# Optimization experiments

Hardware: AMD Instinct MI355X
Metric: run time of the kernel (lower is better)

Reference implementation:

```python
import jax, jax.numpy as jnp
import numpy as np

HIDDEN = 576
N_HEADS = 9
KV_HEADS = 3
HEAD_DIM = HIDDEN // N_HEADS  # 64
ROPE_BASE = 10000.0
B, S = 2, 4096


def rotate_half(x):
    x1, x2 = jnp.split(x, 2, axis=-1)
    return jnp.concatenate((-x2, x1), axis=-1)


def rope_cos_sin(seq_len, dim, base):
    freq = 1.0 / base ** (jnp.arange(0, dim, 2, dtype=jnp.float32) / dim)
    angles = jnp.arange(seq_len, dtype=jnp.float32)[:, None] * freq[None, :]  # [S, dim/2]
    emb = jnp.concatenate((angles, angles), axis=-1)[None]  # [1, S, dim]
    return jnp.cos(emb), jnp.sin(emb)


def setup_inputs() -> dict:
    key = jax.random.key(0)
    kx, kq, kk, kv, ko = jax.random.split(key, 5)
    x = jax.random.normal(kx, (B, S, HIDDEN), dtype=jnp.float32)
    sc = 1.0 / np.sqrt(HIDDEN)
    Wq = jax.random.normal(kq, (HIDDEN, N_HEADS * HEAD_DIM), dtype=jnp.float32) * sc
    Wk = jax.random.normal(kk, (HIDDEN, KV_HEADS * HEAD_DIM), dtype=jnp.float32) * sc
    Wv = jax.random.normal(kv, (HIDDEN, KV_HEADS * HEAD_DIM), dtype=jnp.float32) * sc
    Wo = jax.random.normal(ko, (HIDDEN, HIDDEN), dtype=jnp.float32) * sc
    causal = jnp.where(jnp.tril(jnp.ones((S, S), dtype=bool)), 0.0, -1e9).astype(jnp.float32)
    attention_mask = jnp.broadcast_to(causal[None, None], (B, 1, S, S))
    return {"x": x, "attention_mask": attention_mask, "Wq": Wq, "Wk": Wk, "Wv": Wv, "Wo": Wo}


def reference(x, attention_mask, Wq, Wk, Wv, Wo):
    b, s, _ = x.shape
    n_rep = N_HEADS // KV_HEADS
    # projections -> [b, heads, s, d]
    q = (x @ Wq).reshape(b, s, N_HEADS, HEAD_DIM).transpose(0, 2, 1, 3)
    k = (x @ Wk).reshape(b, s, KV_HEADS, HEAD_DIM).transpose(0, 2, 1, 3)
    v = (x @ Wv).reshape(b, s, KV_HEADS, HEAD_DIM).transpose(0, 2, 1, 3)
    cos, sin = rope_cos_sin(s, HEAD_DIM, ROPE_BASE)
    cos, sin = cos[:, None], sin[:, None]  # unsqueeze head dim -> [1,1,s,d]
    q = q * cos + rotate_half(q) * sin
    k = k * cos + rotate_half(k) * sin
    # repeat_kv expansion
    k = jnp.repeat(k, n_rep, axis=1)
    v = jnp.repeat(v, n_rep, axis=1)
    scores = jnp.einsum('bhqd,bhkd->bhqk', q, k) / jnp.sqrt(jnp.float32(HEAD_DIM))
    scores = scores + attention_mask
    attn = jax.nn.softmax(scores, axis=-1)
    out = jnp.einsum('bhqk,bhkd->bhqd', attn, v)
    out = out.transpose(0, 2, 1, 3).reshape(b, s, HIDDEN)
    return out @ Wo
```

## Files before the change

kernel.cpp:

```cpp
#include <hip/hip_runtime.h>
#include <hip/hip_bf16.h>
#include <math.h>

#define HID 576
#define NHEADS 9
#define KVHEADS 3
#define HD 64
#define SEQ 4096
#define NBATCH 2

typedef __attribute__((ext_vector_type(8))) short short8;
typedef __attribute__((ext_vector_type(4))) float f32x4;
typedef __attribute__((ext_vector_type(16))) float f32x16;
typedef __attribute__((ext_vector_type(4))) unsigned int u32x4;

#define EXP2F(x) exp2f(x)

#define QSCALE 0.18033688011112042f

#define NBH (NBATCH*NHEADS)
#define NPAIR 64

__device__ __forceinline__ unsigned short f2bf(float f){
  unsigned int u = __float_as_uint(f);
  u += 0x7FFFu + ((u >> 16) & 1u);
  return (unsigned short)(u >> 16);
}
__device__ __forceinline__ float bf2f(unsigned short u){
  return __uint_as_float(((unsigned)u) << 16);
}

__device__ __forceinline__ unsigned cvt_pk_bf16(float lo, float hi){
  unsigned r;
  asm("v_cvt_pk_bf16_f32 %0, %1, %2" : "=v"(r) : "v"(lo), "v"(hi));
  return r;
}

__global__ __launch_bounds__(256) void k_cast(const float* __restrict__ x,
                                              unsigned short* __restrict__ xb, int n){
  int i = (blockIdx.x * 256 + threadIdx.x) * 4;
  if (i < n){
    float4 v = *(const float4*)(x + i);
    ushort4 o;
    o.x = f2bf(v.x); o.y = f2bf(v.y); o.z = f2bf(v.z); o.w = f2bf(v.w);
    *(ushort4*)(xb + i) = o;
  }
}

__global__ __launch_bounds__(256) void k_qkv(const unsigned short* __restrict__ xb,
    const float* __restrict__ Wq, const float* __restrict__ Wk, const float* __restrict__ Wv,
    unsigned short* __restrict__ Qo, unsigned short* __restrict__ Ko,
    unsigned short* __restrict__ Vt)
{
  __shared__ unsigned short As[64][40];
  __shared__ unsigned short Bs[64][40];
  const int tn = blockIdx.x;
  const int m0 = blockIdx.y * 64;
  const int t  = threadIdx.x;
  const int w  = t >> 6;
  const int l  = t & 63;
  const int l15 = l & 15, lg = l >> 4;

  const float* W; int nb, ldw;
  if (tn < 9)      { W = Wq; nb = tn * 64;        ldw = 576; }
  else if (tn < 12){ W = Wk; nb = (tn - 9) * 64;  ldw = 192; }
  else             { W = Wv; nb = (tn - 12) * 64; ldw = 192; }

  f32x4 acc[4];
  #pragma unroll
  for (int n = 0; n < 4; ++n){ f32x4 z = {0.f,0.f,0.f,0.f}; acc[n] = z; }

  const int ar = t >> 2, ac = (t & 3) * 8;
  const int bkr = t >> 3, bnc = (t & 7) * 8;

  for (int kt = 0; kt < 18; ++kt){
    const int k0 = kt * 32;
    *(short8*)&As[ar][ac] = *(const short8*)(xb + (m0 + ar) * 576 + k0 + ac);
    {
      const float* src = W + (k0 + bkr) * ldw + nb + bnc;
      float4 v0 = *(const float4*)src;
      float4 v1 = *(const float4*)(src + 4);
      Bs[bnc+0][bkr] = f2bf(v0.x); Bs[bnc+1][bkr] = f2bf(v0.y);
      Bs[bnc+2][bkr] = f2bf(v0.z); Bs[bnc+3][bkr] = f2bf(v0.w);
      Bs[bnc+4][bkr] = f2bf(v1.x); Bs[bnc+5][bkr] = f2bf(v1.y);
      Bs[bnc+6][bkr] = f2bf(v1.z); Bs[bnc+7][bkr] = f2bf(v1.w);
    }
    __syncthreads();
    short8 af = *(const short8*)&As[w*16 + l15][lg*8];
    #pragma unroll
    for (int n = 0; n < 4; ++n){
      short8 bf = *(const short8*)&Bs[n*16 + l15][lg*8];
      acc[n] = __builtin_amdgcn_mfma_f32_16x16x32_bf16(af, bf, acc[n], 0, 0, 0);
    }
    __syncthreads();
  }

  if (tn < 12){
    #pragma unroll
    for (int np = 0; np < 2; ++np){
      const int p = np*16 + l15;
      const float freq = exp2f((float)p * -0.41524101186f);
      #pragma unroll
      for (int reg = 0; reg < 4; ++reg){
        const int grow = m0 + w*16 + lg*4 + reg;
        const int s = grow & (SEQ-1);
        float si, co;
        sincosf((float)s * freq, &si, &co);
        float v0 = acc[np][reg], v1 = acc[np+2][reg];
        acc[np][reg]   = v0*co - v1*si;
        acc[np+2][reg] = v1*co + v0*si;
      }
    }
  }

  if (tn < 9){
    const int h = tn;
    #pragma unroll
    for (int reg = 0; reg < 4; ++reg){
      const int grow = m0 + w*16 + lg*4 + reg;
      const int b = grow >> 12, s = grow & (SEQ-1);
      unsigned short* dst = Qo + ((b*NHEADS + h)*SEQ + s)*64;
      #pragma unroll
      for (int n = 0; n < 4; ++n) dst[n*16 + l15] = f2bf(acc[n][reg] * QSCALE);
    }
  } else if (tn < 12){
    const int h = tn - 9;
    #pragma unroll
    for (int reg = 0; reg < 4; ++reg){
      const int grow = m0 + w*16 + lg*4 + reg;
      const int b = grow >> 12, s = grow & (SEQ-1);
      unsigned short* dst = Ko + ((b*KVHEADS + h)*SEQ + s)*64;
      #pragma unroll
      for (int n = 0; n < 4; ++n) dst[n*16 + l15] = f2bf(acc[n][reg]);
    }
  } else {
    const int h = tn - 12;
    #pragma unroll
    for (int reg = 0; reg < 4; ++reg){
      const int grow = m0 + w*16 + lg*4 + reg;
      const int b = grow >> 12, s = grow & (SEQ-1);
      #pragma unroll
      for (int n = 0; n < 4; ++n)
        Vt[((b*KVHEADS + h)*64 + n*16 + l15)*SEQ + s] = f2bf(acc[n][reg]);
    }
  }
}

__global__ __launch_bounds__(64, 2) void k_attn9(const unsigned short* __restrict__ Q,
    const unsigned short* __restrict__ K, const unsigned short* __restrict__ Vt,
    unsigned short* __restrict__ AO,
    unsigned short* __restrict__ PO, float* __restrict__ Pm, float* __restrict__ Pl,
    int CSP)
{
  int rem = blockIdx.x;
  int j = NPAIR - 1;
  int nch;
  for (;;){
    nch = (2*j + 2 + CSP - 1) / CSP;
    const int cnt = NBH * nch;
    if (rem < cnt || j == 0) break;
    rem -= cnt; --j;
  }
  const int bh = rem / nch;
  const int c  = rem % nch;
  const int s0 = c * CSP;
  const int s1 = min(s0 + CSP, 2*j + 2);
  const bool partial = (nch > 1);
  const int slot = blockIdx.x;

  const int b  = bh / NHEADS, h = bh % NHEADS, kvh = h / 3;
  const int l  = threadIdx.x;
  const int q31 = l & 31, half = l >> 5;
  const int qA0 = j*64, qB0 = j*64 + 32;
  const int myqA = qA0 + q31, myqB = qB0 + q31;

  const unsigned short* QpA = Q + ((size_t)(b*NHEADS + h)*SEQ + qA0 + q31)*HD + half*8;
  const short8 qa0 = *(const short8*)(QpA);
  const short8 qa1 = *(const short8*)(QpA + 16);
  const short8 qa2 = *(const short8*)(QpA + 32);
  const short8 qa3 = *(const short8*)(QpA + 48);
  const unsigned short* QpB = QpA + (size_t)32*HD;
  const short8 qb0 = *(const short8*)(QpB);
  const short8 qb1 = *(const short8*)(QpB + 16);
  const short8 qb2 = *(const short8*)(QpB + 32);
  const short8 qb3 = *(const short8*)(QpB + 48);

  const unsigned short* Kp  = K  + (size_t)(b*KVHEADS + kvh)*SEQ*HD + (size_t)q31*HD + half*8;
  const unsigned short* Vp0 = Vt + (size_t)(b*KVHEADS + kvh)*HD*SEQ + (size_t)q31*SEQ + half*8;
  const unsigned short* Vp1 = Vp0 + (size_t)32*SEQ;

  f32x16 aA0 = {}, aA1 = {}, aB0 = {}, aB1 = {};
  float mA = -3e38f, lsA = 0.f, mB = -3e38f, lsB = 0.f;

  const unsigned short* kp0 = Kp + (size_t)(s0*32)*HD;
  short8 ckf0 = *(const short8*)(kp0);
  short8 ckf1 = *(const short8*)(kp0 + 16);
  short8 ckf2 = *(const short8*)(kp0 + 32);
  short8 ckf3 = *(const short8*)(kp0 + 48);

  for (int s = s0; s < s1; ++s){
    const int ks = s*32;

    short8 vf00 = *(const short8*)(Vp0 + ks);
    short8 vf01 = *(const short8*)(Vp0 + ks + 16);
    short8 vf10 = *(const short8*)(Vp1 + ks);
    short8 vf11 = *(const short8*)(Vp1 + ks + 16);

    __builtin_amdgcn_s_setprio(1);
    f32x16 stA = {}, stB = {};
    stA = __builtin_amdgcn_mfma_f32_32x32x16_bf16(ckf0, qa0, stA, 0,0,0);
    stB = __builtin_amdgcn_mfma_f32_32x32x16_bf16(ckf0, qb0, stB, 0,0,0);
    stA = __builtin_amdgcn_mfma_f32_32x32x16_bf16(ckf1, qa1, stA, 0,0,0);
    stB = __builtin_amdgcn_mfma_f32_32x32x16_bf16(ckf1, qb1, stB, 0,0,0);
    stA = __builtin_amdgcn_mfma_f32_32x32x16_bf16(ckf2, qa2, stA, 0,0,0);
    stB = __builtin_amdgcn_mfma_f32_32x32x16_bf16(ckf2, qb2, stB, 0,0,0);
    stA = __builtin_amdgcn_mfma_f32_32x32x16_bf16(ckf3, qa3, stA, 0,0,0);
    stB = __builtin_amdgcn_mfma_f32_32x32x16_bf16(ckf3, qb3, stB, 0,0,0);
    __builtin_amdgcn_s_setprio(0);

    short8 nkf0, nkf1, nkf2, nkf3;
    const bool more = (s + 1 < s1);
    if (more){
      const unsigned short* kp = Kp + (size_t)(ks + 32)*HD;
      nkf0 = *(const short8*)(kp);
      nkf1 = *(const short8*)(kp + 16);
      nkf2 = *(const short8*)(kp + 32);
      nkf3 = *(const short8*)(kp + 48);
    }

    if (s >= 2*j){
      #pragma unroll
      for (int r = 0; r < 16; ++r){
        const int k = ks + (r & 3) + 8*(r >> 2) + 4*half;
        if (k > myqA) stA[r] = -3e38f;
      }
    }
    if (s == 2*j + 1){
      #pragma unroll
      for (int r = 0; r < 16; ++r){
        const int k = ks + (r & 3) + 8*(r >> 2) + 4*half;
        if (k > myqB) stB[r] = -3e38f;
      }
    }

    {
      float a0 = fmaxf(stA[0], stA[1]),  a1 = fmaxf(stA[2], stA[3]);
      float a2 = fmaxf(stA[4], stA[5]),  a3 = fmaxf(stA[6], stA[7]);
      float a4 = fmaxf(stA[8], stA[9]),  a5 = fmaxf(stA[10], stA[11]);
      float a6 = fmaxf(stA[12], stA[13]),a7 = fmaxf(stA[14], stA[15]);
      float b0 = fmaxf(a0, a1), b1 = fmaxf(a2, a3), b2 = fmaxf(a4, a5), b3 = fmaxf(a6, a7);
      float pmax = fmaxf(fmaxf(b0, b1), fmaxf(b2, b3));
      pmax = fmaxf(pmax, __shfl_xor(pmax, 32));
      if (__any(pmax > mA + 8.0f)){
        const float mnew  = fmaxf(mA, pmax);
        const float alpha = EXP2F(mA - mnew);
        mA = mnew;
        lsA *= alpha;
        #pragma unroll
        for (int r = 0; r < 16; ++r){
          const float ar = __shfl(alpha, (r & 3) + 8*(r >> 2) + 4*half);
          aA0[r] *= ar; aA1[r] *= ar;
        }
      }
      float psum = 0.f;
      #pragma unroll
      for (int r = 0; r < 16; ++r){ stA[r] = EXP2F(stA[r] - mA); psum += stA[r]; }
      psum += __shfl_xor(psum, 32);
      lsA += psum;
    }
    {
      float a0 = fmaxf(stB[0], stB[1]),  a1 = fmaxf(stB[2], stB[3]);
      float a2 = fmaxf(stB[4], stB[5]),  a3 = fmaxf(stB[6], stB[7]);
      float a4 = fmaxf(stB[8], stB[9]),  a5 = fmaxf(stB[10], stB[11]);
      float a6 = fmaxf(stB[12], stB[13]),a7 = fmaxf(stB[14], stB[15]);
      float b0 = fmaxf(a0, a1), b1 = fmaxf(a2, a3), b2 = fmaxf(a4, a5), b3 = fmaxf(a6, a7);
      float pmax = fmaxf(fmaxf(b0, b1), fmaxf(b2, b3));
      pmax = fmaxf(pmax, __shfl_xor(pmax, 32));
      if (__any(pmax > mB + 8.0f)){
        const float mnew  = fmaxf(mB, pmax);
        const float alpha = EXP2F(mB - mnew);
        mB = mnew;
        lsB *= alpha;
        #pragma unroll
        for (int r = 0; r < 16; ++r){
          const float ar = __shfl(alpha, (r & 3) + 8*(r >> 2) + 4*half);
          aB0[r] *= ar; aB1[r] *= ar;
        }
      }
      float psum = 0.f;
      #pragma unroll
      for (int r = 0; r < 16; ++r){ stB[r] = EXP2F(stB[r] - mB); psum += stB[r]; }
      psum += __shfl_xor(psum, 32);
      lsB += psum;
    }

    union { u32x4 u; short8 s; } paA0, paA1, paB0, paB1;
    {
      unsigned cA = cvt_pk_bf16(stA[0], stA[1]);
      unsigned cB = cvt_pk_bf16(stA[2], stA[3]);
      unsigned cC = cvt_pk_bf16(stA[4], stA[5]);
      unsigned cD = cvt_pk_bf16(stA[6], stA[7]);
      asm("v_permlane32_swap_b32 %0, %1" : "+v"(cA), "+v"(cC));
      asm("v_permlane32_swap_b32 %0, %1" : "+v"(cB), "+v"(cD));
      paA0.u[0] = cA; paA0.u[1] = cB; paA0.u[2] = cC; paA0.u[3] = cD;
      unsigned eA = cvt_pk_bf16(stA[8],  stA[9]);
      unsigned eB = cvt_pk_bf16(stA[10], stA[11]);
      unsigned eC = cvt_pk_bf16(stA[12], stA[13]);
      unsigned eD = cvt_pk_bf16(stA[14], stA[15]);
      asm("v_permlane32_swap_b32 %0, %1" : "+v"(eA), "+v"(eC));
      asm("v_permlane32_swap_b32 %0, %1" : "+v"(eB), "+v"(eD));
      paA1.u[0] = eA; paA1.u[1] = eB; paA1.u[2] = eC; paA1.u[3] = eD;
    }
    {
      unsigned cA = cvt_pk_bf16(stB[0], stB[1]);
      unsigned cB = cvt_pk_bf16(stB[2], stB[3]);
      unsigned cC = cvt_pk_bf16(stB[4], stB[5]);
      unsigned cD = cvt_pk_bf16(stB[6], stB[7]);
      asm("v_permlane32_swap_b32 %0, %1" : "+v"(cA), "+v"(cC));
      asm("v_permlane32_swap_b32 %0, %1" : "+v"(cB), "+v"(cD));
      paB0.u[0] = cA; paB0.u[1] = cB; paB0.u[2] = cC; paB0.u[3] = cD;
      unsigned eA = cvt_pk_bf16(stB[8],  stB[9]);
      unsigned eB = cvt_pk_bf16(stB[10], stB[11]);
      unsigned eC = cvt_pk_bf16(stB[12], stB[13]);
      unsigned eD = cvt_pk_bf16(stB[14], stB[15]);
      asm("v_permlane32_swap_b32 %0, %1" : "+v"(eA), "+v"(eC));
      asm("v_permlane32_swap_b32 %0, %1" : "+v"(eB), "+v"(eD));
      paB1.u[0] = eA; paB1.u[1] = eB; paB1.u[2] = eC; paB1.u[3] = eD;
    }

    __builtin_amdgcn_s_setprio(1);
    aA0 = __builtin_amdgcn_mfma_f32_32x32x16_bf16(paA0.s, vf00, aA0, 0,0,0);
    aB0 = __builtin_amdgcn_mfma_f32_32x32x16_bf16(paB0.s, vf00, aB0, 0,0,0);
    aA0 = __builtin_amdgcn_mfma_f32_32x32x16_bf16(paA1.s, vf01, aA0, 0,0,0);
    aB0 = __builtin_amdgcn_mfma_f32_32x32x16_bf16(paB1.s, vf01, aB0, 0,0,0);
    aA1 = __builtin_amdgcn_mfma_f32_32x32x16_bf16(paA0.s, vf10, aA1, 0,0,0);
    aB1 = __builtin_amdgcn_mfma_f32_32x32x16_bf16(paB0.s, vf10, aB1, 0,0,0);
    aA1 = __builtin_amdgcn_mfma_f32_32x32x16_bf16(paA1.s, vf11, aA1, 0,0,0);
    aB1 = __builtin_amdgcn_mfma_f32_32x32x16_bf16(paB1.s, vf11, aB1, 0,0,0);
    __builtin_amdgcn_s_setprio(0);

    if (more){ ckf0 = nkf0; ckf1 = nkf1; ckf2 = nkf2; ckf3 = nkf3; }
  }

  if (partial){
    unsigned short* PA = PO + (size_t)(slot*2)   * (32*64);
    unsigned short* PB = PO + (size_t)(slot*2+1) * (32*64);
    #pragma unroll
    for (int r = 0; r < 16; ++r){
      const int rq = (r & 3) + 8*(r >> 2) + 4*half;
      PA[rq*64 + q31]      = f2bf(aA0[r]);
      PA[rq*64 + q31 + 32] = f2bf(aA1[r]);
      PB[rq*64 + q31]      = f2bf(aB0[r]);
      PB[rq*64 + q31 + 32] = f2bf(aB1[r]);
    }
    if (half == 0){
      Pm[(size_t)(slot*2)*32 + q31]   = mA;
      Pl[(size_t)(slot*2)*32 + q31]   = lsA;
      Pm[(size_t)(slot*2+1)*32 + q31] = mB;
      Pl[(size_t)(slot*2+1)*32 + q31] = lsB;
    }
  } else {
    const float liA = 1.0f / lsA, liB = 1.0f / lsB;
    #pragma unroll
    for (int r = 0; r < 16; ++r){
      const int rq = (r & 3) + 8*(r >> 2) + 4*half;
      const float la = __shfl(liA, rq), lb = __shfl(liB, rq);
      const size_t baseA = ((size_t)(b*SEQ + qA0 + rq))*576 + h*64 + q31;
      AO[baseA]      = f2bf(aA0[r] * la);
      AO[baseA + 32] = f2bf(aA1[r] * la);
      const size_t baseB = ((size_t)(b*SEQ + qB0 + rq))*576 + h*64 + q31;
      AO[baseB]      = f2bf(aB0[r] * lb);
      AO[baseB + 32] = f2bf(aB1[r] * lb);
    }
  }
}

__global__ __launch_bounds__(256) void k_comb3(const unsigned short* __restrict__ PO,
    const float* __restrict__ Pm, const float* __restrict__ Pl,
    unsigned short* __restrict__ AO, int CSP)
{
  const int blk = blockIdx.x;
  const int mp = blk >> 1, X = blk & 1;
  const int j  = (NPAIR-1) - mp / NBH;
  const int bh = mp % NBH;
  const int nch = (2*j + 2 + CSP - 1) / CSP;
  int pbase = 0;
  for (int j2 = NPAIR-1; j2 > j; --j2) pbase += NBH * ((2*j2 + 2 + CSP - 1) / CSP);
  pbase += bh * nch;

  const int b = bh / NHEADS, h = bh % NHEADS;
  const int t = threadIdx.x;
  const int row = t >> 3;
  const int dg  = (t & 7) * 8;
  const int q0 = j*64 + 32*X;

  float M = -3e38f;
  for (int cc = 0; cc < nch; ++cc)
    M = fmaxf(M, Pm[(size_t)((pbase + cc)*2 + X)*32 + row]);

  float ls = 0.f;
  float o0=0.f,o1=0.f,o2=0.f,o3=0.f,o4=0.f,o5=0.f,o6=0.f,o7=0.f;
  for (int cc = 0; cc < nch; ++cc){
    const int sid = (pbase + cc)*2 + X;
    const float wc = exp2f(Pm[(size_t)sid*32 + row] - M);
    ls += Pl[(size_t)sid*32 + row] * wc;
    const short8 po = *(const short8*)(PO + (size_t)sid*(32*64) + row*64 + dg);
    o0 += bf2f((unsigned short)po[0]) * wc;
    o1 += bf2f((unsigned short)po[1]) * wc;
    o2 += bf2f((unsigned short)po[2]) * wc;
    o3 += bf2f((unsigned short)po[3]) * wc;
    o4 += bf2f((unsigned short)po[4]) * wc;
    o5 += bf2f((unsigned short)po[5]) * wc;
    o6 += bf2f((unsigned short)po[6]) * wc;
    o7 += bf2f((unsigned short)po[7]) * wc;
  }
  const float li = 1.0f / ls;
  ushort4 w0, w1;
  w0.x = f2bf(o0*li); w0.y = f2bf(o1*li); w0.z = f2bf(o2*li); w0.w = f2bf(o3*li);
  w1.x = f2bf(o4*li); w1.y = f2bf(o5*li); w1.z = f2bf(o6*li); w1.w = f2bf(o7*li);
  unsigned short* dst = AO + ((size_t)(b*SEQ + q0 + row))*576 + h*64 + dg;
  *(ushort4*)(dst)     = w0;
  *(ushort4*)(dst + 4) = w1;
}

__global__ __launch_bounds__(256) void k_oproj(const unsigned short* __restrict__ AO,
    const float* __restrict__ Wo, float* __restrict__ out)
{
  __shared__ unsigned short As[64][40];
  __shared__ unsigned short Bs[64][40];
  const int tn = blockIdx.x;
  const int m0 = blockIdx.y * 64;
  const int t  = threadIdx.x;
  const int w  = t >> 6;
  const int l  = t & 63;
  const int l15 = l & 15, lg = l >> 4;
  const int nb = tn * 64;

  f32x4 acc[4];
  #pragma unroll
  for (int n = 0; n < 4; ++n){ f32x4 z = {0.f,0.f,0.f,0.f}; acc[n] = z; }

  const int ar = t >> 2, ac = (t & 3) * 8;
  const int bkr = t >> 3, bnc = (t & 7) * 8;

  for (int kt = 0; kt < 18; ++kt){
    const int k0 = kt * 32;
    *(short8*)&As[ar][ac] = *(const short8*)(AO + (m0 + ar) * 576 + k0 + ac);
    {
      const float* src = Wo + (k0 + bkr) * 576 + nb + bnc;
      float4 v0 = *(const float4*)src;
      float4 v1 = *(const float4*)(src + 4);
      Bs[bnc+0][bkr] = f2bf(v0.x); Bs[bnc+1][bkr] = f2bf(v0.y);
      Bs[bnc+2][bkr] = f2bf(v0.z); Bs[bnc+3][bkr] = f2bf(v0.w);
      Bs[bnc+4][bkr] = f2bf(v1.x); Bs[bnc+5][bkr] = f2bf(v1.y);
      Bs[bnc+6][bkr] = f2bf(v1.z); Bs[bnc+7][bkr] = f2bf(v1.w);
    }
    __syncthreads();
    short8 af = *(const short8*)&As[w*16 + l15][lg*8];
    #pragma unroll
    for (int n = 0; n < 4; ++n){
      short8 bf = *(const short8*)&Bs[n*16 + l15][lg*8];
      acc[n] = __builtin_amdgcn_mfma_f32_16x16x32_bf16(af, bf, acc[n], 0, 0, 0);
    }
    __syncthreads();
  }

  #pragma unroll
  for (int reg = 0; reg < 4; ++reg){
    const int grow = m0 + w*16 + lg*4 + reg;
    float* dst = out + (size_t)grow * 576 + nb;
    #pragma unroll
    for (int n = 0; n < 4; ++n) dst[n*16 + l15] = acc[n][reg];
  }
}

extern "C" void kernel_launch(void* const* d_in, const int* in_sizes, int n_in,
                              void* d_out, int out_size, void* d_ws, size_t ws_size,
                              hipStream_t stream) {
  const float* x  = (const float*)d_in[0];
  const float* Wq = (const float*)d_in[2];
  const float* Wk = (const float*)d_in[3];
  const float* Wv = (const float*)d_in[4];
  const float* Wo = (const float*)d_in[5];
  float* out = (float*)d_out;

  char* ws = (char*)d_ws;
  const size_t XB_BYTES = (size_t)NBATCH*SEQ*HID*2;
  const size_t Q_BYTES  = (size_t)NBATCH*NHEADS*SEQ*HD*2;
  const size_t K_BYTES  = (size_t)NBATCH*KVHEADS*SEQ*HD*2;
  const size_t V_BYTES  = K_BYTES;
  const size_t BASE     = XB_BYTES + Q_BYTES + K_BYTES + V_BYTES;

  int CSP = 256;
  size_t S = 0;
  {
    const int cands[3] = {20, 40, 64};
    for (int ci = 0; ci < 3; ++ci){
      const int cs = cands[ci];
      size_t s2 = 0;
      for (int j = 0; j < NPAIR; ++j) s2 += (size_t)((2*j + 2 + cs - 1) / cs);
      s2 *= NBH;
      const size_t need = BASE + s2*2*(32*64)*2 + 2*(s2*2*32*4);
      if (ws_size >= need){ CSP = cs; break; }
    }
    size_t s3 = 0;
    for (int j = 0; j < NPAIR; ++j) s3 += (size_t)((2*j + 2 + CSP - 1) / CSP);
    S = s3 * NBH;
  }
  const size_t PO_BYTES = S*2*(32*64)*2;
  const size_t PM_BYTES = S*2*32*4;
  const int jmin = CSP/2;
  const int mpairs = (jmin < NPAIR) ? (NPAIR - jmin)*NBH : 0;

  unsigned short* xb = (unsigned short*)ws;
  unsigned short* Q  = (unsigned short*)(ws + XB_BYTES);
  unsigned short* K  = (unsigned short*)(ws + XB_BYTES + Q_BYTES);
  unsigned short* Vt = (unsigned short*)(ws + XB_BYTES + Q_BYTES + K_BYTES);
  unsigned short* PO = (unsigned short*)(ws + BASE);
  float* Pm = (float*)(ws + BASE + PO_BYTES);
  float* Pl = (float*)(ws + BASE + PO_BYTES + PM_BYTES);
  unsigned short* AO = xb;

  hipLaunchKernelGGL(k_cast, dim3((NBATCH*SEQ*HID)/1024), dim3(256), 0, stream,
                     x, xb, NBATCH*SEQ*HID);
  hipLaunchKernelGGL(k_qkv, dim3(15, (NBATCH*SEQ)/64), dim3(256), 0, stream,
                     xb, Wq, Wk, Wv, Q, K, Vt);
  hipLaunchKernelGGL(k_attn9, dim3((unsigned)S), dim3(64), 0, stream,
                     Q, K, Vt, AO, PO, Pm, Pl, CSP);
  if (mpairs > 0)
    hipLaunchKernelGGL(k_comb3, dim3(mpairs*2), dim3(256), 0, stream, PO, Pm, Pl, AO, CSP);
  hipLaunchKernelGGL(k_oproj, dim3(9, (NBATCH*SEQ)/64), dim3(256), 0, stream,
                     AO, Wo, out);
}
```

Measured before the change: 201.0 us.

## Pre-transpose weights to bf16, fuse x cast into QKV, pack attention waves

A new kernel converts all four weight matrices once per call into transposed bf16 copies, so the QKV and output-projection GEMMs load B tiles with plain vector copies instead of scattered per-element f32-to-bf16 stores into shared memory. The separate x-to-bf16 cast kernel is removed; the QKV kernel now reads f32 x directly and converts it with packed bf16 instructions. The attention kernel is relaunched with four independent wavefronts per 256-thread block instead of one wave per block, cutting block count and scheduling overhead. The cost is an extra weight-transpose launch with strided, uncoalesced reads, and more workspace memory.

After: 488.5 us. 143% more time.

```diff
diff --git a/kernel.cpp b/kernel.cpp
--- a/kernel.cpp
+++ b/kernel.cpp
@@ -36,19 +36,28 @@
   return r;
 }
 
-__global__ __launch_bounds__(256) void k_cast(const float* __restrict__ x,
-                                              unsigned short* __restrict__ xb, int n){
-  int i = (blockIdx.x * 256 + threadIdx.x) * 4;
-  if (i < n){
-    float4 v = *(const float4*)(x + i);
-    ushort4 o;
-    o.x = f2bf(v.x); o.y = f2bf(v.y); o.z = f2bf(v.z); o.w = f2bf(v.w);
-    *(ushort4*)(xb + i) = o;
-  }
-}
-
-__global__ __launch_bounds__(256) void k_qkv(const unsigned short* __restrict__ xb,
-    const float* __restrict__ Wq, const float* __restrict__ Wk, const float* __restrict__ Wv,
+__global__ __launch_bounds__(64) void k_prepw(const float* __restrict__ Wq,
+    const float* __restrict__ Wk, const float* __restrict__ Wv, const float* __restrict__ Wo,
+    unsigned short* __restrict__ WTq, unsigned short* __restrict__ WTk,
+    unsigned short* __restrict__ WTv, unsigned short* __restrict__ WTo)
+{
+  const int r = blockIdx.x;
+  const float* W; unsigned short* WT; int N, n;
+  if (r < 576)      { W = Wq; WT = WTq; N = 576; n = r; }
+  else if (r < 768) { W = Wk; WT = WTk; N = 192; n = r - 576; }
+  else if (r < 960) { W = Wv; WT = WTv; N = 192; n = r - 768; }
+  else              { W = Wo; WT = WTo; N = 576; n = r - 960; }
+  const int t = threadIdx.x;
+  #pragma unroll
+  for (int kk = 0; kk < 9; ++kk){
+    const int k = kk*64 + t;
+    WT[(size_t)n*576 + k] = f2bf(W[(size_t)k*N + n]);
+  }
+}
+
+__global__ __launch_bounds__(256) void k_qkv(const float* __restrict__ x,
+    const unsigned short* __restrict__ WTq, const unsigned short* __restrict__ WTk,
+    const unsigned short* __restrict__ WTv,
     unsigned short* __restrict__ Qo, unsigned short* __restrict__ Ko,
     unsigned short* __restrict__ Vt)
 {
@@ -61,29 +70,29 @@
   const int l  = t & 63;
   const int l15 = l & 15, lg = l >> 4;
 
-  const float* W; int nb, ldw;
-  if (tn < 9)      { W = Wq; nb = tn * 64;        ldw = 576; }
-  else if (tn < 12){ W = Wk; nb = (tn - 9) * 64;  ldw = 192; }
-  else             { W = Wv; nb = (tn - 12) * 64; ldw = 192; }
+  const unsigned short* WT; int nb;
+  if (tn < 9)      { WT = WTq; nb = tn * 64; }
+  else if (tn < 12){ WT = WTk; nb = (tn - 9) * 64; }
+  else             { WT = WTv; nb = (tn - 12) * 64; }
 
   f32x4 acc[4];
   #pragma unroll
   for (int n = 0; n < 4; ++n){ f32x4 z = {0.f,0.f,0.f,0.f}; acc[n] = z; }
 
   const int ar = t >> 2, ac = (t & 3) * 8;
-  const int bkr = t >> 3, bnc = (t & 7) * 8;
+  const int br = t >> 2, bc = (t & 3) * 8;
 
   for (int kt = 0; kt < 18; ++kt){
     const int k0 = kt * 32;
-    *(short8*)&As[ar][ac] = *(const short8*)(xb + (m0 + ar) * 576 + k0 + ac);
     {
-      const float* src = W + (k0 + bkr) * ldw + nb + bnc;
-      float4 v0 = *(const float4*)src;
-      float4 v1 = *(const float4*)(src + 4);
-      Bs[bnc+0][bkr] = f2bf(v0.x); Bs[bnc+1][bkr] = f2bf(v0.y);
-      Bs[bnc+2][bkr] = f2bf(v0.z); Bs[bnc+3][bkr] = f2bf(v0.w);
-      Bs[bnc+4][bkr] = f2bf(v1.x); Bs[bnc+5][bkr] = f2bf(v1.y);
-      Bs[bnc+6][bkr] = f2bf(v1.z); Bs[bnc+7][bkr] = f2bf(v1.w);
+      const float* srcA = x + (size_t)(m0 + ar)*576 + k0 + ac;
+      float4 a0 = *(const float4*)srcA;
+      float4 a1 = *(const float4*)(srcA + 4);
+      u32x4 pk;
+      pk[0] = cvt_pk_bf16(a0.x, a0.y); pk[1] = cvt_pk_bf16(a0.z, a0.w);
+      pk[2] = cvt_pk_bf16(a1.x, a1.y); pk[3] = cvt_pk_bf16(a1.z, a1.w);
+      *(u32x4*)&As[ar][ac] = pk;
+      *(short8*)&Bs[br][bc] = *(const short8*)(WT + (size_t)(nb + br)*576 + k0 + bc);
     }
     __syncthreads();
     short8 af = *(const short8*)&As[w*16 + l15][lg*8];
@@ -146,13 +155,16 @@
   }
 }
 
-__global__ __launch_bounds__(64, 2) void k_attn9(const unsigned short* __restrict__ Q,
+__global__ __launch_bounds__(256, 4) void k_attn10(const unsigned short* __restrict__ Q,
     const unsigned short* __restrict__ K, const unsigned short* __restrict__ Vt,
     unsigned short* __restrict__ AO,
     unsigned short* __restrict__ PO, float* __restrict__ Pm, float* __restrict__ Pl,
-    int CSP)
+    int CSP, int Stotal)
 {
-  int rem = blockIdx.x;
+  const int slot = blockIdx.x * 4 + (threadIdx.x >> 6);
+  if (slot >= Stotal) return;
+
+  int rem = slot;
   int j = NPAIR - 1;
   int nch;
   for (;;){
@@ -166,10 +178,9 @@
   const int s0 = c * CSP;
   const int s1 = min(s0 + CSP, 2*j + 2);
   const bool partial = (nch > 1);
-  const int slot = blockIdx.x;
 
   const int b  = bh / NHEADS, h = bh % NHEADS, kvh = h / 3;
-  const int l  = threadIdx.x;
+  const int l  = threadIdx.x & 63;
   const int q31 = l & 31, half = l >> 5;
   const int qA0 = j*64, qB0 = j*64 + 32;
   const int myqA = qA0 + q31, myqB = qB0 + q31;
@@ -424,7 +435,7 @@
 }
 
 __global__ __launch_bounds__(256) void k_oproj(const unsigned short* __restrict__ AO,
-    const float* __restrict__ Wo, float* __restrict__ out)
+    const unsigned short* __restrict__ WoT, float* __restrict__ out)
 {
   __shared__ unsigned short As[64][40];
   __shared__ unsigned short Bs[64][40];
@@ -441,20 +452,11 @@
   for (int n = 0; n < 4; ++n){ f32x4 z = {0.f,0.f,0.f,0.f}; acc[n] = z; }
 
   const int ar = t >> 2, ac = (t & 3) * 8;
-  const int bkr = t >> 3, bnc = (t & 7) * 8;
 
   for (int kt = 0; kt < 18; ++kt){
     const int k0 = kt * 32;
-    *(short8*)&As[ar][ac] = *(const short8*)(AO + (m0 + ar) * 576 + k0 + ac);
-    {
-      const float* src = Wo + (k0 + bkr) * 576 + nb + bnc;
-      float4 v0 = *(const float4*)src;
-      float4 v1 = *(const float4*)(src + 4);
-      Bs[bnc+0][bkr] = f2bf(v0.x); Bs[bnc+1][bkr] = f2bf(v0.y);
-      Bs[bnc+2][bkr] = f2bf(v0.z); Bs[bnc+3][bkr] = f2bf(v0.w);
-      Bs[bnc+4][bkr] = f2bf(v1.x); Bs[bnc+5][bkr] = f2bf(v1.y);
-      Bs[bnc+6][bkr] = f2bf(v1.z); Bs[bnc+7][bkr] = f2bf(v1.w);
-    }
+    *(short8*)&As[ar][ac] = *(const short8*)(AO + (size_t)(m0 + ar)*576 + k0 + ac);
+    *(short8*)&Bs[ar][ac] = *(const short8*)(WoT + (size_t)(nb + ar)*576 + k0 + ac);
     __syncthreads();
     short8 af = *(const short8*)&As[w*16 + l15][lg*8];
     #pragma unroll
@@ -485,11 +487,14 @@
   float* out = (float*)d_out;
 
   char* ws = (char*)d_ws;
-  const size_t XB_BYTES = (size_t)NBATCH*SEQ*HID*2;
-  const size_t Q_BYTES  = (size_t)NBATCH*NHEADS*SEQ*HD*2;
-  const size_t K_BYTES  = (size_t)NBATCH*KVHEADS*SEQ*HD*2;
-  const size_t V_BYTES  = K_BYTES;
-  const size_t BASE     = XB_BYTES + Q_BYTES + K_BYTES + V_BYTES;
+  const size_t AO_BYTES  = (size_t)NBATCH*SEQ*HID*2;
+  const size_t Q_BYTES   = (size_t)NBATCH*NHEADS*SEQ*HD*2;
+  const size_t K_BYTES   = (size_t)NBATCH*KVHEADS*SEQ*HD*2;
+  const size_t V_BYTES   = K_BYTES;
+  const size_t WTQ_BYTES = (size_t)576*576*2;
+  const size_t WTK_BYTES = (size_t)192*576*2;
+  const size_t WT_BYTES  = WTQ_BYTES*2 + WTK_BYTES*2;
+  const size_t BASE      = AO_BYTES + Q_BYTES + K_BYTES + V_BYTES + WT_BYTES;
 
   int CSP = 256;
   size_t S = 0;
@@ -512,23 +517,26 @@
   const int jmin = CSP/2;
   const int mpairs = (jmin < NPAIR) ? (NPAIR - jmin)*NBH : 0;
 
-  unsigned short* xb = (unsigned short*)ws;
-  unsigned short* Q  = (unsigned short*)(ws + XB_BYTES);
-  unsigned short* K  = (unsigned short*)(ws + XB_BYTES + Q_BYTES);
-  unsigned short* Vt = (unsigned short*)(ws + XB_BYTES + Q_BYTES + K_BYTES);
-  unsigned short* PO = (unsigned short*)(ws + BASE);
+  unsigned short* AO  = (unsigned short*)ws;
+  unsigned short* Q   = (unsigned short*)(ws + AO_BYTES);
+  unsigned short* K   = (unsigned short*)(ws + AO_BYTES + Q_BYTES);
+  unsigned short* Vt  = (unsigned short*)(ws + AO_BYTES + Q_BYTES + K_BYTES);
+  unsigned short* WTq = (unsigned short*)(ws + AO_BYTES + Q_BYTES + K_BYTES + V_BYTES);
+  unsigned short* WTk = WTq + 576*576;
+  unsigned short* WTv = WTk + 192*576;
+  unsigned short* WTo = WTv + 192*576;
+  unsigned short* PO  = (unsigned short*)(ws + BASE);
   float* Pm = (float*)(ws + BASE + PO_BYTES);
   float* Pl = (float*)(ws + BASE + PO_BYTES + PM_BYTES);
-  unsigned short* AO = xb;
-
-  hipLaunchKernelGGL(k_cast, dim3((NBATCH*SEQ*HID)/1024), dim3(256), 0, stream,
-                     x, xb, NBATCH*SEQ*HID);
+
+  hipLaunchKernelGGL(k_prepw, dim3(1536), dim3(64), 0, stream,
+                     Wq, Wk, Wv, Wo, WTq, WTk, WTv, WTo);
   hipLaunchKernelGGL(k_qkv, dim3(15, (NBATCH*SEQ)/64), dim3(256), 0, stream,
-                     xb, Wq, Wk, Wv, Q, K, Vt);
-  hipLaunchKernelGGL(k_attn9, dim3((unsigned)S), dim3(64), 0, stream,
-                     Q, K, Vt, AO, PO, Pm, Pl, CSP);
+                     x, WTq, WTk, WTv, Q, K, Vt);
+  hipLaunchKernelGGL(k_attn10, dim3((unsigned)((S + 3) / 4)), dim3(256), 0, stream,
+                     Q, K, Vt, AO, PO, Pm, Pl, CSP, (int)S);
   if (mpairs > 0)
     hipLaunchKernelGGL(k_comb3, dim3(mpairs*2), dim3(256), 0, stream, PO, Pm, Pl, AO, CSP);
   hipLaunchKernelGGL(k_oproj, dim3(9, (NBATCH*SEQ)/64), dim3(256), 0, stream,
-                     AO, Wo, out);
-}
+                     AO, WTo, out);
+}
```
